# Performance work log

Hardware: AMD Instinct MI355X
Metric: run time of the kernel (lower is better)

## Reference

```python
import jax, jax.numpy as jnp
import numpy as np

TEMPERATURE = 0.5
EPS = 1e-8  # torch.nn.CosineSimilarity eps


def setup_inputs() -> dict:
    key = jax.random.key(0)
    k1, k2 = jax.random.split(key)
    B, D = 4096, 128
    z_i = jax.random.normal(k1, (B, D), dtype=jnp.float32)
    z_j = jax.random.normal(k2, (B, D), dtype=jnp.float32)
    return {"z_i": z_i, "z_j": z_j}


def _nt_xent(z_i, z_j, temperature=TEMPERATURE):
    B = z_i.shape[0]
    reps = jnp.concatenate([z_i, z_j], axis=0)                 # [N, D], N = 2B
    norms = jnp.maximum(jnp.linalg.norm(reps, axis=1, keepdims=True), EPS)
    zn = reps / norms                                          # normalize once
    sim = jnp.matmul(zn, zn.T) / temperature                   # [N, N] via GEMM
    exp_sim = jnp.exp(sim)
    # positives: offset-diagonals +B and -B
    idx = jnp.arange(B)
    sim_i_j = exp_sim[idx, idx + B]
    sim_j_i = exp_sim[idx + B, idx]
    pos_pairs = jnp.concatenate([sim_i_j, sim_j_i], axis=0)    # [N]
    sim_self = jnp.diagonal(exp_sim)                           # [N]
    denominator = jnp.sum(exp_sim, axis=1) - sim_self          # [N]
    itemized_loss = -jnp.log(pos_pairs / denominator)
    return jnp.mean(itemized_loss)


def reference(z_i, z_j):
    return _nt_xent(z_i, z_j)
```

## Files before the change

### kernel.cpp

```cpp
#include <hip/hip_runtime.h>
#include <hip/hip_bf16.h>

#define B_ROWS 4096
#define N_ROWS 8192
#define D 128
#define SCALE 2.885390081777927f
#define LN2 0.6931471805599453f

#define RB 256
#define CSPLIT 512
#define CHUNK 64
#define NCHUNK (CSPLIT / CHUNK)

typedef __attribute__((ext_vector_type(8))) short bf16x8;
typedef __attribute__((ext_vector_type(4))) float f32x4;

__device__ inline unsigned short f32_to_bf16_rne(float f) {
    unsigned int u = __float_as_uint(f);
    u += 0x7fffu + ((u >> 16) & 1u);
    return (unsigned short)(u >> 16);
}
__device__ inline float bf16s_to_f32(short s) {
    unsigned int u = ((unsigned int)(unsigned short)s) << 16;
    return __uint_as_float(u);
}

__global__ void k_normalize(const float* __restrict__ z_i,
                            const float* __restrict__ z_j,
                            unsigned short* __restrict__ zn,
                            float* __restrict__ denom,
                            float* __restrict__ out) {
    if (blockIdx.x < 32) denom[blockIdx.x * 256 + threadIdx.x] = 0.f;
    if (blockIdx.x == 0 && threadIdx.x == 0) out[0] = 0.f;

    int row  = blockIdx.x * 4 + (threadIdx.x >> 6);
    int lane = threadIdx.x & 63;
    const float* src = (row < B_ROWS) ? (z_i + (size_t)row * D)
                                      : (z_j + (size_t)(row - B_ROWS) * D);
    float2 v = ((const float2*)src)[lane];
    float ss = v.x * v.x + v.y * v.y;
    #pragma unroll
    for (int m = 1; m < 64; m <<= 1) ss += __shfl_xor(ss, m);
    float rinv = 1.0f / fmaxf(sqrtf(ss), 1e-8f);
    ushort2 o;
    o.x = f32_to_bf16_rne(v.x * rinv);
    o.y = f32_to_bf16_rne(v.y * rinv);
    ((ushort2*)(zn + (size_t)row * D))[lane] = o;
}

__global__ __launch_bounds__(256, 2)
void k_simsum(const unsigned short* __restrict__ zn,
              float* __restrict__ denom) {
    __shared__ unsigned short sB[2 * CHUNK * 16 * 8];
    const int tid  = threadIdx.x;
    const int wave = tid >> 6;
    const int lane = tid & 63;
    const int l15  = lane & 15;
    const int quad = lane >> 4;
    const int m0   = blockIdx.x * RB + wave * 64;

    bf16x8 A[4][4];
    #pragma unroll
    for (int rt = 0; rt < 4; ++rt)
        #pragma unroll
        for (int kb = 0; kb < 4; ++kb)
            A[rt][kb] = *(const bf16x8*)(zn + (size_t)(m0 + rt * 16 + l15) * D + kb * 32 + quad * 8);

    float rs[4][4];
    #pragma unroll
    for (int rt = 0; rt < 4; ++rt)
        #pragma unroll
        for (int j = 0; j < 4; ++j) rs[rt][j] = 0.f;

    const int c_base = blockIdx.y * CSPLIT;

    float4 st[4];
    #pragma unroll
    for (int p = 0; p < 4; ++p) {
        int i = tid + p * 256, c = i >> 4, j = i & 15;
        st[p] = *(const float4*)(zn + (size_t)(c_base + c) * D + j * 8);
    }

    for (int cb = 0; cb < NCHUNK; ++cb) {
        unsigned short* buf = sB + (cb & 1) * (CHUNK * 16 * 8);
        #pragma unroll
        for (int p = 0; p < 4; ++p) {
            int i = tid + p * 256, c = i >> 4, j = i & 15;
            int piece = c * 16 + (j ^ (c & 7));
            *(float4*)(buf + piece * 8) = st[p];
        }
        __syncthreads();

        if (cb + 1 < NCHUNK) {
            #pragma unroll
            for (int p = 0; p < 4; ++p) {
                int i = tid + p * 256, c = i >> 4, j = i & 15;
                st[p] = *(const float4*)(zn + (size_t)(c_base + (cb + 1) * CHUNK + c) * D + j * 8);
            }
        }

        #pragma unroll
        for (int t = 0; t < 4; ++t) {
            bf16x8 b[4];
            #pragma unroll
            for (int kb = 0; kb < 4; ++kb) {
                int c = t * 16 + l15;
                int piece = c * 16 + ((kb * 4 + quad) ^ (c & 7));
                b[kb] = *(const bf16x8*)(buf + piece * 8);
            }
            f32x4 acc[4];
            #pragma unroll
            for (int rt = 0; rt < 4; ++rt) acc[rt] = (f32x4){0.f, 0.f, 0.f, 0.f};
            #pragma unroll
            for (int kb = 0; kb < 4; ++kb)
                #pragma unroll
                for (int rt = 0; rt < 4; ++rt)
                    acc[rt] = __builtin_amdgcn_mfma_f32_16x16x32_bf16(A[rt][kb], b[kb], acc[rt], 0, 0, 0);
            #pragma unroll
            for (int rt = 0; rt < 4; ++rt)
                #pragma unroll
                for (int j = 0; j < 4; ++j)
                    rs[rt][j] += __builtin_amdgcn_exp2f(acc[rt][j] * SCALE);
        }
    }

    #pragma unroll
    for (int rt = 0; rt < 4; ++rt)
        #pragma unroll
        for (int j = 0; j < 4; ++j) {
            float v = rs[rt][j];
            v += __shfl_xor(v, 1);
            v += __shfl_xor(v, 2);
            v += __shfl_xor(v, 4);
            v += __shfl_xor(v, 8);
            rs[rt][j] = v;
        }
    if (l15 == 0) {
        #pragma unroll
        for (int rt = 0; rt < 4; ++rt)
            #pragma unroll
            for (int j = 0; j < 4; ++j)
                atomicAdd(&denom[m0 + rt * 16 + quad * 4 + j], rs[rt][j]);
    }
}

__global__ void k_finalize(const unsigned short* __restrict__ zn,
                           const float* __restrict__ denom,
                           float* __restrict__ out) {
    int i = blockIdx.x * blockDim.x + threadIdx.x;
    int p = (i + B_ROWS) & (N_ROWS - 1);
    const unsigned short* zi = zn + (size_t)i * D;
    const unsigned short* zp = zn + (size_t)p * D;
    float self_dot = 0.f, pos_dot = 0.f;
    #pragma unroll
    for (int c = 0; c < D / 8; ++c) {
        bf16x8 a = *(const bf16x8*)(zi + c * 8);
        bf16x8 b = *(const bf16x8*)(zp + c * 8);
        #pragma unroll
        for (int j = 0; j < 8; ++j) {
            float av = bf16s_to_f32(a[j]);
            float bv = bf16s_to_f32(b[j]);
            self_dot += av * av;
            pos_dot  += av * bv;
        }
    }
    float dnm  = denom[i] - __builtin_amdgcn_exp2f(self_dot * SCALE);
    float loss = __builtin_amdgcn_logf(dnm) * LN2 - pos_dot * 2.0f;

    float v = loss;
    #pragma unroll
    for (int m = 1; m < 64; m <<= 1) v += __shfl_xor(v, m);
    __shared__ float ws[4];
    int wave = threadIdx.x >> 6;
    if ((threadIdx.x & 63) == 0) ws[wave] = v;
    __syncthreads();
    if (threadIdx.x == 0) {
        float s = ws[0] + ws[1] + ws[2] + ws[3];
        atomicAdd(out, s * (1.0f / (float)N_ROWS));
    }
}

extern "C" void kernel_launch(void* const* d_in, const int* in_sizes, int n_in,
                              void* d_out, int out_size, void* d_ws, size_t ws_size,
                              hipStream_t stream) {
    const float* z_i = (const float*)d_in[0];
    const float* z_j = (const float*)d_in[1];
    float* out = (float*)d_out;

    unsigned short* zn = (unsigned short*)d_ws;
    float* denom = (float*)((char*)d_ws + (size_t)N_ROWS * D * 2);

    k_normalize<<<N_ROWS / 4, 256, 0, stream>>>(z_i, z_j, zn, denom, out);
    k_simsum<<<dim3(N_ROWS / RB, N_ROWS / CSPLIT), 256, 0, stream>>>(zn, denom);
    k_finalize<<<N_ROWS / 256, 256, 0, stream>>>(zn, denom, out);
}
```

Before: 94.95 us.

## Exploit similarity matrix symmetry by computing only upper-triangular tiles

The similarity sum kernel now computes only the upper-triangular set of 128x128 tiles, including the diagonal tiles. Each off-diagonal tile's exponentials are added both to its row sums and, via a shared-memory column reduction, to the transposed tile's row sums. This roughly halves the MFMA and exp work, because sim is symmetric. The cost is more atomics per block, a column reduction through LDS with an extra sync, smaller tiles, and no double-buffered prefetch of column data.

```diff
diff --git a/kernel.cpp b/kernel.cpp
--- a/kernel.cpp
+++ b/kernel.cpp
@@ -7,10 +7,9 @@
 #define SCALE 2.885390081777927f
 #define LN2 0.6931471805599453f
 
-#define RB 256
-#define CSPLIT 512
-#define CHUNK 64
-#define NCHUNK (CSPLIT / CHUNK)
+#define TB 128
+#define NB (N_ROWS / TB)
+#define NBLK (NB * (NB / 2) + NB / 2)
 
 typedef __attribute__((ext_vector_type(8))) short bf16x8;
 typedef __attribute__((ext_vector_type(4))) float f32x4;
@@ -51,81 +50,91 @@
 __global__ __launch_bounds__(256, 2)
 void k_simsum(const unsigned short* __restrict__ zn,
               float* __restrict__ denom) {
-    __shared__ unsigned short sB[2 * CHUNK * 16 * 8];
+    __shared__ unsigned short sB[TB * 16 * 8];
+    __shared__ float csum[4][TB];
+
+    int t = blockIdx.x;
+    int bx, by;
+    if (t < NB * (NB / 2)) { bx = t & (NB - 1); by = t >> 6; }
+    else                   { bx = t - NB * (NB / 2); by = NB / 2; }
+    const int bi   = bx;
+    const int bj   = (bx + by) & (NB - 1);
+    const bool diag = (by == 0);
+
     const int tid  = threadIdx.x;
     const int wave = tid >> 6;
     const int lane = tid & 63;
     const int l15  = lane & 15;
     const int quad = lane >> 4;
-    const int m0   = blockIdx.x * RB + wave * 64;
-
-    bf16x8 A[4][4];
-    #pragma unroll
-    for (int rt = 0; rt < 4; ++rt)
+
+    const int r0 = bi * TB + wave * 32;
+    const int c0 = bj * TB;
+
+    float4 st[8];
+    #pragma unroll
+    for (int p = 0; p < 8; ++p) {
+        int i = tid + p * 256, c = i >> 4, j = i & 15;
+        st[p] = *(const float4*)(zn + (size_t)(c0 + c) * D + j * 8);
+    }
+
+    bf16x8 A[2][4];
+    #pragma unroll
+    for (int rt = 0; rt < 2; ++rt)
         #pragma unroll
         for (int kb = 0; kb < 4; ++kb)
-            A[rt][kb] = *(const bf16x8*)(zn + (size_t)(m0 + rt * 16 + l15) * D + kb * 32 + quad * 8);
-
-    float rs[4][4];
-    #pragma unroll
-    for (int rt = 0; rt < 4; ++rt)
+            A[rt][kb] = *(const bf16x8*)(zn + (size_t)(r0 + rt * 16 + l15) * D + kb * 32 + quad * 8);
+
+    #pragma unroll
+    for (int p = 0; p < 8; ++p) {
+        int i = tid + p * 256, c = i >> 4, j = i & 15;
+        int piece = c * 16 + (j ^ (c & 7));
+        *(float4*)(sB + piece * 8) = st[p];
+    }
+
+    float rs[2][4];
+    #pragma unroll
+    for (int rt = 0; rt < 2; ++rt)
         #pragma unroll
         for (int j = 0; j < 4; ++j) rs[rt][j] = 0.f;
 
-    const int c_base = blockIdx.y * CSPLIT;
-
-    float4 st[4];
-    #pragma unroll
-    for (int p = 0; p < 4; ++p) {
-        int i = tid + p * 256, c = i >> 4, j = i & 15;
-        st[p] = *(const float4*)(zn + (size_t)(c_base + c) * D + j * 8);
-    }
-
-    for (int cb = 0; cb < NCHUNK; ++cb) {
-        unsigned short* buf = sB + (cb & 1) * (CHUNK * 16 * 8);
-        #pragma unroll
-        for (int p = 0; p < 4; ++p) {
-            int i = tid + p * 256, c = i >> 4, j = i & 15;
-            int piece = c * 16 + (j ^ (c & 7));
-            *(float4*)(buf + piece * 8) = st[p];
-        }
-        __syncthreads();
-
-        if (cb + 1 < NCHUNK) {
+    __syncthreads();
+
+    #pragma unroll
+    for (int ct = 0; ct < TB / 16; ++ct) {
+        bf16x8 b[4];
+        #pragma unroll
+        for (int kb = 0; kb < 4; ++kb) {
+            int c = ct * 16 + l15;
+            int piece = c * 16 + ((kb * 4 + quad) ^ (c & 7));
+            b[kb] = *(const bf16x8*)(sB + piece * 8);
+        }
+        f32x4 acc[2];
+        #pragma unroll
+        for (int rt = 0; rt < 2; ++rt) acc[rt] = (f32x4){0.f, 0.f, 0.f, 0.f};
+        #pragma unroll
+        for (int kb = 0; kb < 4; ++kb)
             #pragma unroll
-            for (int p = 0; p < 4; ++p) {
-                int i = tid + p * 256, c = i >> 4, j = i & 15;
-                st[p] = *(const float4*)(zn + (size_t)(c_base + (cb + 1) * CHUNK + c) * D + j * 8);
+            for (int rt = 0; rt < 2; ++rt)
+                acc[rt] = __builtin_amdgcn_mfma_f32_16x16x32_bf16(A[rt][kb], b[kb], acc[rt], 0, 0, 0);
+
+        float cs = 0.f;
+        #pragma unroll
+        for (int rt = 0; rt < 2; ++rt)
+            #pragma unroll
+            for (int j = 0; j < 4; ++j) {
+                float e = __builtin_amdgcn_exp2f(acc[rt][j] * SCALE);
+                rs[rt][j] += e;
+                cs += e;
             }
-        }
-
-        #pragma unroll
-        for (int t = 0; t < 4; ++t) {
-            bf16x8 b[4];
-            #pragma unroll
-            for (int kb = 0; kb < 4; ++kb) {
-                int c = t * 16 + l15;
-                int piece = c * 16 + ((kb * 4 + quad) ^ (c & 7));
-                b[kb] = *(const bf16x8*)(buf + piece * 8);
-            }
-            f32x4 acc[4];
-            #pragma unroll
-            for (int rt = 0; rt < 4; ++rt) acc[rt] = (f32x4){0.f, 0.f, 0.f, 0.f};
-            #pragma unroll
-            for (int kb = 0; kb < 4; ++kb)
-                #pragma unroll
-                for (int rt = 0; rt < 4; ++rt)
-                    acc[rt] = __builtin_amdgcn_mfma_f32_16x16x32_bf16(A[rt][kb], b[kb], acc[rt], 0, 0, 0);
-            #pragma unroll
-            for (int rt = 0; rt < 4; ++rt)
-                #pragma unroll
-                for (int j = 0; j < 4; ++j)
-                    rs[rt][j] += __builtin_amdgcn_exp2f(acc[rt][j] * SCALE);
-        }
-    }
-
-    #pragma unroll
-    for (int rt = 0; rt < 4; ++rt)
+        if (!diag) {
+            cs += __shfl_xor(cs, 16);
+            cs += __shfl_xor(cs, 32);
+            if (quad == 0) csum[wave][ct * 16 + l15] = cs;
+        }
+    }
+
+    #pragma unroll
+    for (int rt = 0; rt < 2; ++rt)
         #pragma unroll
         for (int j = 0; j < 4; ++j) {
             float v = rs[rt][j];
@@ -137,10 +146,18 @@
         }
     if (l15 == 0) {
         #pragma unroll
-        for (int rt = 0; rt < 4; ++rt)
+        for (int rt = 0; rt < 2; ++rt)
             #pragma unroll
             for (int j = 0; j < 4; ++j)
-                atomicAdd(&denom[m0 + rt * 16 + quad * 4 + j], rs[rt][j]);
+                atomicAdd(&denom[r0 + rt * 16 + quad * 4 + j], rs[rt][j]);
+    }
+
+    if (!diag) {
+        __syncthreads();
+        if (tid < TB) {
+            float s = csum[0][tid] + csum[1][tid] + csum[2][tid] + csum[3][tid];
+            atomicAdd(&denom[c0 + tid], s);
+        }
     }
 }
 
@@ -191,6 +208,6 @@
     float* denom = (float*)((char*)d_ws + (size_t)N_ROWS * D * 2);
 
     k_normalize<<<N_ROWS / 4, 256, 0, stream>>>(z_i, z_j, zn, denom, out);
-    k_simsum<<<dim3(N_ROWS / RB, N_ROWS / CSPLIT), 256, 0, stream>>>(zn, denom);
+    k_simsum<<<NBLK, 256, 0, stream>>>(zn, denom);
     k_finalize<<<N_ROWS / 256, 256, 0, stream>>>(zn, denom, out);
 }
```

After: 83.98 us. 1.13x faster.
